# Kernel tuning notes

Measured on AMD Instinct MI355X. Metric: run time of the kernel, lower is better.

The kernel has to match this reference:

```python
import jax, jax.numpy as jnp
import numpy as np

N, D, E, H, K = 16384, 256, 8, 512, 2


def setup_inputs() -> dict:
    key = jax.random.key(0)
    ks = jax.random.split(key, 5)
    inputs = jax.random.normal(ks[0], (N, D), dtype=jnp.float32)
    Wg = jax.random.normal(ks[1], (D, E), dtype=jnp.float32) * 0.05
    w1 = jax.random.normal(ks[2], (E, D, H), dtype=jnp.float32) * 0.05
    b1 = jnp.zeros((E, H), dtype=jnp.float32)
    w2 = jax.random.normal(ks[3], (E, H, D), dtype=jnp.float32) * 0.05
    b2 = jnp.zeros((E, D), dtype=jnp.float32)
    return {"inputs": inputs, "Wg": Wg, "w1": w1, "b1": b1, "w2": w2, "b2": b2}


def reference(inputs, Wg, w1, b1, w2, b2):
    # gate + top-k routing (softmax over the selected logits only, as in the torch code)
    gate_logits = inputs @ Wg                       # [N, E]
    topw, topi = jax.lax.top_k(gate_logits, K)      # [N, K]
    topw = jax.nn.softmax(topw.astype(jnp.float32), axis=1).astype(inputs.dtype)
    # combine weights scattered back into a dense [N, E] matrix (dispatch/combine)
    combine = jnp.zeros((N, E), dtype=inputs.dtype)
    combine = combine.at[jnp.arange(N)[:, None], topi].add(topw)  # [N, E]
    # expert MLP (Linear -> GELU(exact) -> Linear), computed per expert and
    # combined with the sparse routing weights (pool='sum')
    h = jax.nn.gelu(jnp.einsum('nd,edh->neh', inputs, w1) + b1[None], approximate=False)  # [N,E,H]
    y = jnp.einsum('neh,ehd->ned', h, w2) + b2[None]                                      # [N,E,D]
    return jnp.einsum('ne,ned->nd', combine, y)                                           # [N,D]
```

## Files before the change

### kernel.cpp

```cpp
#include <hip/hip_runtime.h>

#define NTOK 16384
#define DIM 256
#define NEXP 8
#define HID 512
#define CAP 5120
#define CSTRIDE 16

typedef unsigned short ushort_t;
typedef short bf16x8 __attribute__((ext_vector_type(8)));
typedef float f32x4 __attribute__((ext_vector_type(4)));

static __device__ __forceinline__ ushort_t f2bf(float f) {
    unsigned int u = __float_as_uint(f);
    unsigned int r = (u + 0x7FFFu + ((u >> 16) & 1u)) >> 16;
    return (ushort_t)r;
}
static __device__ __forceinline__ float bf2f(ushort_t u) {
    unsigned int x = ((unsigned int)u) << 16;
    return __uint_as_float(x);
}
static __device__ __forceinline__ float gelu_fast(float v) {
    float v2 = v * v;
    float u = v * __builtin_fmaf(v2, -0.1029407079f, -2.3022090196f);
    float e = __builtin_amdgcn_exp2f(u);
    return v * __builtin_amdgcn_rcpf(1.0f + e);
}

__global__ void k_transpose(const float* __restrict__ w1, const float* __restrict__ w2,
                            ushort_t* __restrict__ w1t, ushort_t* __restrict__ w2t,
                            int* __restrict__ counts) {
    __shared__ ushort_t tile[64][72];
    if (blockIdx.x == 0 && threadIdx.x < NEXP * CSTRIDE) counts[threadIdx.x] = 0;
    int b = blockIdx.x;
    const float* src; ushort_t* dst; int R, C, e, t;
    if (b < 256) { e = b >> 5; t = b & 31; src = w1; dst = w1t + e * DIM * HID; R = DIM; C = HID; }
    else { b -= 256; e = b >> 5; t = b & 31; src = w2; dst = w2t + e * DIM * HID; R = HID; C = DIM; }
    size_t ebase = (size_t)e * DIM * HID;
    int tilesC = C >> 6;
    int rt = t / tilesC, ct = t % tilesC;
    for (int i = 0; i < 16; i++) {
        int flat = i * 256 + threadIdx.x;
        int lr = flat >> 6, lc = flat & 63;
        tile[lr][lc] = f2bf(src[ebase + (size_t)(rt * 64 + lr) * C + ct * 64 + lc]);
    }
    __syncthreads();
    for (int i = 0; i < 16; i++) {
        int flat = i * 256 + threadIdx.x;
        int lr = flat >> 6, lc = flat & 63;
        dst[(ct * 64 + lr) * R + rt * 64 + lc] = tile[lc][lr];
    }
}

__global__ void k_router(const float* __restrict__ X, const float* __restrict__ Wg,
                         int* counts, int* tok_list, int* inv_idx, float* inv_w,
                         ushort_t* __restrict__ Xb) {
    __shared__ float xs[32][257];
    __shared__ float lg[32][8];
    __shared__ int te0[32], te1[32], lo0[32], lo1[32];
    __shared__ float tw0[32], tw1[32];
    __shared__ int lcnt[NEXP], gbase[NEXP];
    int tid = threadIdx.x;
    int tok0 = blockIdx.x * 32;
    if (tid < NEXP) lcnt[tid] = 0;
    for (int i = 0; i < 4; i++) {
        int flat = i * 256 + tid;
        int r = flat >> 5, c8 = (flat & 31) << 3;
        const float* row = X + (size_t)(tok0 + r) * DIM + c8;
        float4 a = *(const float4*)row;
        float4 b = *(const float4*)(row + 4);
        xs[r][c8 + 0] = a.x; xs[r][c8 + 1] = a.y; xs[r][c8 + 2] = a.z; xs[r][c8 + 3] = a.w;
        xs[r][c8 + 4] = b.x; xs[r][c8 + 5] = b.y; xs[r][c8 + 6] = b.z; xs[r][c8 + 7] = b.w;
    }
    __syncthreads();
    for (int i = 0; i < 4; i++) {
        int flat = i * 256 + tid;
        int r = flat >> 5, c8 = (flat & 31) << 3;
        ushort_t pk[8];
#pragma unroll
        for (int j = 0; j < 8; j++) pk[j] = f2bf(xs[r][c8 + j]);
        *(int4*)(Xb + (size_t)(tok0 + r) * DIM + c8) = *(const int4*)pk;
    }
    int tl = tid & 31, ex = tid >> 5;
    float acc = 0.f;
    for (int d = 0; d < DIM; d++) acc += xs[tl][d] * Wg[d * NEXP + ex];
    lg[tl][ex] = acc;
    __syncthreads();
    if (tid < 32) {
        float best = -1e30f; int bi = 0;
#pragma unroll
        for (int e = 0; e < NEXP; e++) { float v = lg[tid][e]; if (v > best) { best = v; bi = e; } }
        float best2 = -1e30f; int bi2 = 0;
#pragma unroll
        for (int e = 0; e < NEXP; e++) { if (e == bi) continue; float v = lg[tid][e]; if (v > best2) { best2 = v; bi2 = e; } }
        float ed = __expf(best2 - best);
        te0[tid] = bi; te1[tid] = bi2;
        tw0[tid] = 1.0f / (1.0f + ed);
        tw1[tid] = ed / (1.0f + ed);
        lo0[tid] = atomicAdd(&lcnt[bi], 1);
        lo1[tid] = atomicAdd(&lcnt[bi2], 1);
    }
    __syncthreads();
    if (tid < NEXP) gbase[tid] = atomicAdd(&counts[tid * CSTRIDE], lcnt[tid]);
    __syncthreads();
    if (tid < 32) {
        int token = tok0 + tid;
        int e0 = te0[tid], e1 = te1[tid];
        int p0 = gbase[e0] + lo0[tid]; if (p0 >= CAP) p0 = CAP - 1;
        int p1 = gbase[e1] + lo1[tid]; if (p1 >= CAP) p1 = CAP - 1;
        tok_list[e0 * CAP + p0] = token;
        tok_list[e1 * CAP + p1] = token;
        inv_idx[token * 2]     = (e0 << 16) | p0;  inv_w[token * 2]     = tw0[tid];
        inv_idx[token * 2 + 1] = (e1 << 16) | p1;  inv_w[token * 2 + 1] = tw1[tid];
    }
}

__launch_bounds__(512, 4)
__global__ void k_mlp1(const ushort_t* __restrict__ Xb, const ushort_t* __restrict__ w1t,
                       const float* __restrict__ b1,
                       const int* __restrict__ counts, const int* __restrict__ tok_list,
                       ushort_t* __restrict__ hb) {
    __shared__ ushort_t B1[128 * 264];
    int b = blockIdx.x;
    int e = b / 40;
    int tile = b % 40;
    int count = counts[e * CSTRIDE];
    if (count > CAP) count = CAP;
    int t0 = tile * 128;
    if (t0 >= count) return;

    int tid = threadIdx.x;
    int w = tid >> 6, l = tid & 63, ln = l & 15, q = l >> 4;

    int arow = t0 + 16 * w + ln;
    int ci = (arow < count) ? arow : (count - 1);
    int atok = tok_list[e * CAP + ci];
    const ushort_t* xrow = Xb + (size_t)atok * DIM;
    bf16x8 xf[8];
#pragma unroll
    for (int ks = 0; ks < 8; ks++)
        xf[ks] = *(const bf16x8*)(xrow + ks * 32 + q * 8);

    const ushort_t* w1te = w1t + (size_t)e * DIM * HID;
    size_t hrowbase = ((size_t)e * CAP + t0 + 16 * w + ln) * HID;

    for (int hq = 0; hq < 4; hq++) {
        __syncthreads();
#pragma unroll
        for (int i = 0; i < 8; i++) {
            int flat = i * 512 + tid;
            int hr = flat >> 5, c8 = (flat & 31) << 3;
            *(int4*)(B1 + hr * 264 + c8) = *(const int4*)(w1te + (size_t)(hq * 128 + hr) * DIM + c8);
        }
        __syncthreads();

        f32x4 zf = {0.f, 0.f, 0.f, 0.f};
        f32x4 acc[8];
#pragma unroll
        for (int i = 0; i < 8; i++) acc[i] = zf;
#pragma unroll
        for (int ks = 0; ks < 8; ks++) {
            bf16x8 xk = xf[ks];
#pragma unroll
            for (int cf = 0; cf < 8; cf++) {
                bf16x8 wfr = *(const bf16x8*)(B1 + (cf * 16 + ln) * 264 + ks * 32 + q * 8);
                acc[cf] = __builtin_amdgcn_mfma_f32_16x16x32_bf16(wfr, xk, acc[cf], 0, 0, 0);
            }
        }
#pragma unroll
        for (int cf = 0; cf < 8; cf++) {
            float4 bv = *(const float4*)(b1 + e * HID + hq * 128 + cf * 16 + q * 4);
            ushort4 pk;
            pk.x = f2bf(gelu_fast(acc[cf][0] + bv.x));
            pk.y = f2bf(gelu_fast(acc[cf][1] + bv.y));
            pk.z = f2bf(gelu_fast(acc[cf][2] + bv.z));
            pk.w = f2bf(gelu_fast(acc[cf][3] + bv.w));
            *(ushort4*)(hb + hrowbase + hq * 128 + cf * 16 + q * 4) = pk;
        }
    }
}

__launch_bounds__(512, 4)
__global__ void k_mlp2(const ushort_t* __restrict__ hb, const ushort_t* __restrict__ w2t,
                       const float* __restrict__ b2,
                       const int* __restrict__ counts, ushort_t* __restrict__ yb) {
    __shared__ ushort_t B2[64 * 520];
    int b = blockIdx.x;
    int e = b / 40;
    int tile = b % 40;
    int count = counts[e * CSTRIDE];
    if (count > CAP) count = CAP;
    int t0 = tile * 128;
    if (t0 >= count) return;

    int tid = threadIdx.x;
    int w = tid >> 6, l = tid & 63, ln = l & 15, q = l >> 4;

    int arow = t0 + 16 * w + ln;
    int ci = (arow < count) ? arow : (count - 1);
    const ushort_t* hrow = hb + ((size_t)e * CAP + ci) * HID;
    bf16x8 af[16];
#pragma unroll
    for (int ks = 0; ks < 16; ks++)
        af[ks] = *(const bf16x8*)(hrow + ks * 32 + q * 8);

    const ushort_t* w2te = w2t + (size_t)e * DIM * HID;
    size_t yrowbase = ((size_t)e * CAP + t0 + 16 * w + ln) * DIM;

    for (int dq = 0; dq < 4; dq++) {
        __syncthreads();
#pragma unroll
        for (int i = 0; i < 8; i++) {
            int flat = i * 512 + tid;
            int dr = flat >> 6, c8 = (flat & 63) << 3;
            *(int4*)(B2 + dr * 520 + c8) = *(const int4*)(w2te + (size_t)(dq * 64 + dr) * HID + c8);
        }
        __syncthreads();

        f32x4 zf = {0.f, 0.f, 0.f, 0.f};
        f32x4 acc[4];
#pragma unroll
        for (int i = 0; i < 4; i++) acc[i] = zf;
#pragma unroll
        for (int ks = 0; ks < 16; ks++) {
            bf16x8 hk = af[ks];
#pragma unroll
            for (int cf = 0; cf < 4; cf++) {
                bf16x8 wfr = *(const bf16x8*)(B2 + (cf * 16 + ln) * 520 + ks * 32 + q * 8);
                acc[cf] = __builtin_amdgcn_mfma_f32_16x16x32_bf16(wfr, hk, acc[cf], 0, 0, 0);
            }
        }
#pragma unroll
        for (int cf = 0; cf < 4; cf++) {
            float4 bv = *(const float4*)(b2 + e * DIM + dq * 64 + cf * 16 + q * 4);
            ushort4 pk;
            pk.x = f2bf(acc[cf][0] + bv.x);
            pk.y = f2bf(acc[cf][1] + bv.y);
            pk.z = f2bf(acc[cf][2] + bv.z);
            pk.w = f2bf(acc[cf][3] + bv.w);
            *(ushort4*)(yb + yrowbase + dq * 64 + cf * 16 + q * 4) = pk;
        }
    }
}

__global__ void k_combine(const ushort_t* __restrict__ yb, const int* __restrict__ inv_idx,
                          const float* __restrict__ inv_w, float* __restrict__ out) {
    int tid = threadIdx.x;
    int n = blockIdx.x * 8 + (tid >> 5);
    int l32 = tid & 31, c8 = l32 << 3;
    int i0 = inv_idx[2 * n], i1 = inv_idx[2 * n + 1];
    float w0 = inv_w[2 * n], w1 = inv_w[2 * n + 1];
    size_t r0 = (size_t)(i0 >> 16) * CAP + (i0 & 0xFFFF);
    size_t r1 = (size_t)(i1 >> 16) * CAP + (i1 & 0xFFFF);
    int4 v0 = *(const int4*)(yb + r0 * DIM + c8);
    int4 v1 = *(const int4*)(yb + r1 * DIM + c8);
    ushort_t* p0 = (ushort_t*)&v0;
    ushort_t* p1 = (ushort_t*)&v1;
    float4 oa, ob;
    oa.x = w0 * bf2f(p0[0]) + w1 * bf2f(p1[0]);
    oa.y = w0 * bf2f(p0[1]) + w1 * bf2f(p1[1]);
    oa.z = w0 * bf2f(p0[2]) + w1 * bf2f(p1[2]);
    oa.w = w0 * bf2f(p0[3]) + w1 * bf2f(p1[3]);
    ob.x = w0 * bf2f(p0[4]) + w1 * bf2f(p1[4]);
    ob.y = w0 * bf2f(p0[5]) + w1 * bf2f(p1[5]);
    ob.z = w0 * bf2f(p0[6]) + w1 * bf2f(p1[6]);
    ob.w = w0 * bf2f(p0[7]) + w1 * bf2f(p1[7]);
    float4* op = (float4*)(out + (size_t)n * DIM + c8);
    op[0] = oa; op[1] = ob;
}

extern "C" void kernel_launch(void* const* d_in, const int* in_sizes, int n_in,
                              void* d_out, int out_size, void* d_ws, size_t ws_size,
                              hipStream_t stream) {
    const float* X  = (const float*)d_in[0];
    const float* Wg = (const float*)d_in[1];
    const float* w1 = (const float*)d_in[2];
    const float* b1 = (const float*)d_in[3];
    const float* w2 = (const float*)d_in[4];
    const float* b2 = (const float*)d_in[5];

    char* ws = (char*)d_ws;
    size_t off = 0;
    int* counts = (int*)(ws + off);        off = 1024;
    int* tok_list = (int*)(ws + off);      off += (size_t)NEXP * CAP * 4;
    int* inv_idx = (int*)(ws + off);       off += (size_t)NTOK * 2 * 4;
    float* inv_w = (float*)(ws + off);     off += (size_t)NTOK * 2 * 4;
    ushort_t* w1t = (ushort_t*)(ws + off); off += (size_t)NEXP * DIM * HID * 2;
    ushort_t* w2t = (ushort_t*)(ws + off); off += (size_t)NEXP * DIM * HID * 2;
    ushort_t* Xb = (ushort_t*)(ws + off);  off += (size_t)NTOK * DIM * 2;
    ushort_t* hb = (ushort_t*)(ws + off);  off += (size_t)NEXP * CAP * HID * 2;
    ushort_t* yb = (ushort_t*)(ws + off);  off += (size_t)NEXP * CAP * DIM * 2;

    k_transpose<<<512, 256, 0, stream>>>(w1, w2, w1t, w2t, counts);
    k_router<<<512, 256, 0, stream>>>(X, Wg, counts, tok_list, inv_idx, inv_w, Xb);
    k_mlp1<<<NEXP * 40, 512, 0, stream>>>(Xb, w1t, b1, counts, tok_list, hb);
    k_mlp2<<<NEXP * 40, 512, 0, stream>>>(hb, w2t, b2, counts, yb);
    k_combine<<<2048, 256, 0, stream>>>(yb, inv_idx, inv_w, (float*)d_out);
}
```

Measured before the change: 183.8 us.

## Split MLP kernels across output-column chunks for more, smaller blocks

Each MLP block now handles 64 token rows and a single 64-wide (mlp1) or 32-wide (mlp2) output column chunk, with the chunk index taken from the grid. This replaces the in-block loop over four column chunks. Grid size grows from 320 to 5120 blocks of 256 threads, with smaller shared tiles, to raise occupancy and spread load across CUs. The cost is that each block reloads its activation rows, so gathered X and h reads are repeated 8 times, and more blocks exit early.

```diff
diff --git a/kernel.cpp b/kernel.cpp
--- a/kernel.cpp
+++ b/kernel.cpp
@@ -115,18 +115,19 @@
     }
 }
 
-__launch_bounds__(512, 4)
+__launch_bounds__(256, 4)
 __global__ void k_mlp1(const ushort_t* __restrict__ Xb, const ushort_t* __restrict__ w1t,
                        const float* __restrict__ b1,
                        const int* __restrict__ counts, const int* __restrict__ tok_list,
                        ushort_t* __restrict__ hb) {
-    __shared__ ushort_t B1[128 * 264];
+    __shared__ ushort_t B1[64 * 264];
     int b = blockIdx.x;
-    int e = b / 40;
-    int tile = b % 40;
+    int e = b / 640;
+    int rem = b % 640;
+    int hq = rem / 80, tile = rem % 80;
     int count = counts[e * CSTRIDE];
     if (count > CAP) count = CAP;
-    int t0 = tile * 128;
+    int t0 = tile * 64;
     if (t0 >= count) return;
 
     int tid = threadIdx.x;
@@ -141,56 +142,53 @@
     for (int ks = 0; ks < 8; ks++)
         xf[ks] = *(const bf16x8*)(xrow + ks * 32 + q * 8);
 
-    const ushort_t* w1te = w1t + (size_t)e * DIM * HID;
-    size_t hrowbase = ((size_t)e * CAP + t0 + 16 * w + ln) * HID;
-
-    for (int hq = 0; hq < 4; hq++) {
-        __syncthreads();
-#pragma unroll
-        for (int i = 0; i < 8; i++) {
-            int flat = i * 512 + tid;
-            int hr = flat >> 5, c8 = (flat & 31) << 3;
-            *(int4*)(B1 + hr * 264 + c8) = *(const int4*)(w1te + (size_t)(hq * 128 + hr) * DIM + c8);
+    const ushort_t* w1te = w1t + (size_t)e * DIM * HID + (size_t)hq * 64 * DIM;
+#pragma unroll
+    for (int i = 0; i < 8; i++) {
+        int flat = i * 256 + tid;
+        int hr = flat >> 5, c8 = (flat & 31) << 3;
+        *(int4*)(B1 + hr * 264 + c8) = *(const int4*)(w1te + hr * DIM + c8);
+    }
+    __syncthreads();
+
+    f32x4 zf = {0.f, 0.f, 0.f, 0.f};
+    f32x4 acc[4];
+#pragma unroll
+    for (int i = 0; i < 4; i++) acc[i] = zf;
+#pragma unroll
+    for (int ks = 0; ks < 8; ks++) {
+        bf16x8 xk = xf[ks];
+#pragma unroll
+        for (int cf = 0; cf < 4; cf++) {
+            bf16x8 wfr = *(const bf16x8*)(B1 + (cf * 16 + ln) * 264 + ks * 32 + q * 8);
+            acc[cf] = __builtin_amdgcn_mfma_f32_16x16x32_bf16(wfr, xk, acc[cf], 0, 0, 0);
         }
-        __syncthreads();
-
-        f32x4 zf = {0.f, 0.f, 0.f, 0.f};
-        f32x4 acc[8];
-#pragma unroll
-        for (int i = 0; i < 8; i++) acc[i] = zf;
-#pragma unroll
-        for (int ks = 0; ks < 8; ks++) {
-            bf16x8 xk = xf[ks];
-#pragma unroll
-            for (int cf = 0; cf < 8; cf++) {
-                bf16x8 wfr = *(const bf16x8*)(B1 + (cf * 16 + ln) * 264 + ks * 32 + q * 8);
-                acc[cf] = __builtin_amdgcn_mfma_f32_16x16x32_bf16(wfr, xk, acc[cf], 0, 0, 0);
-            }
-        }
-#pragma unroll
-        for (int cf = 0; cf < 8; cf++) {
-            float4 bv = *(const float4*)(b1 + e * HID + hq * 128 + cf * 16 + q * 4);
-            ushort4 pk;
-            pk.x = f2bf(gelu_fast(acc[cf][0] + bv.x));
-            pk.y = f2bf(gelu_fast(acc[cf][1] + bv.y));
-            pk.z = f2bf(gelu_fast(acc[cf][2] + bv.z));
-            pk.w = f2bf(gelu_fast(acc[cf][3] + bv.w));
-            *(ushort4*)(hb + hrowbase + hq * 128 + cf * 16 + q * 4) = pk;
-        }
-    }
-}
-
-__launch_bounds__(512, 4)
+    }
+    size_t hrowbase = ((size_t)e * CAP + arow) * HID + hq * 64;
+#pragma unroll
+    for (int cf = 0; cf < 4; cf++) {
+        float4 bv = *(const float4*)(b1 + e * HID + hq * 64 + cf * 16 + q * 4);
+        ushort4 pk;
+        pk.x = f2bf(gelu_fast(acc[cf][0] + bv.x));
+        pk.y = f2bf(gelu_fast(acc[cf][1] + bv.y));
+        pk.z = f2bf(gelu_fast(acc[cf][2] + bv.z));
+        pk.w = f2bf(gelu_fast(acc[cf][3] + bv.w));
+        *(ushort4*)(hb + hrowbase + cf * 16 + q * 4) = pk;
+    }
+}
+
+__launch_bounds__(256, 4)
 __global__ void k_mlp2(const ushort_t* __restrict__ hb, const ushort_t* __restrict__ w2t,
                        const float* __restrict__ b2,
                        const int* __restrict__ counts, ushort_t* __restrict__ yb) {
-    __shared__ ushort_t B2[64 * 520];
+    __shared__ ushort_t B2[32 * 520];
     int b = blockIdx.x;
-    int e = b / 40;
-    int tile = b % 40;
+    int e = b / 640;
+    int rem = b % 640;
+    int dq = rem / 80, tile = rem % 80;
     int count = counts[e * CSTRIDE];
     if (count > CAP) count = CAP;
-    int t0 = tile * 128;
+    int t0 = tile * 64;
     if (t0 >= count) return;
 
     int tid = threadIdx.x;
@@ -204,42 +202,37 @@
     for (int ks = 0; ks < 16; ks++)
         af[ks] = *(const bf16x8*)(hrow + ks * 32 + q * 8);
 
-    const ushort_t* w2te = w2t + (size_t)e * DIM * HID;
-    size_t yrowbase = ((size_t)e * CAP + t0 + 16 * w + ln) * DIM;
-
-    for (int dq = 0; dq < 4; dq++) {
-        __syncthreads();
-#pragma unroll
-        for (int i = 0; i < 8; i++) {
-            int flat = i * 512 + tid;
-            int dr = flat >> 6, c8 = (flat & 63) << 3;
-            *(int4*)(B2 + dr * 520 + c8) = *(const int4*)(w2te + (size_t)(dq * 64 + dr) * HID + c8);
+    const ushort_t* w2te = w2t + (size_t)e * DIM * HID + (size_t)dq * 32 * HID;
+#pragma unroll
+    for (int i = 0; i < 8; i++) {
+        int flat = i * 256 + tid;
+        int dr = flat >> 6, c8 = (flat & 63) << 3;
+        *(int4*)(B2 + dr * 520 + c8) = *(const int4*)(w2te + dr * HID + c8);
+    }
+    __syncthreads();
+
+    f32x4 zf = {0.f, 0.f, 0.f, 0.f};
+    f32x4 acc[2];
+    acc[0] = zf; acc[1] = zf;
+#pragma unroll
+    for (int ks = 0; ks < 16; ks++) {
+        bf16x8 hk = af[ks];
+#pragma unroll
+        for (int cf = 0; cf < 2; cf++) {
+            bf16x8 wfr = *(const bf16x8*)(B2 + (cf * 16 + ln) * 520 + ks * 32 + q * 8);
+            acc[cf] = __builtin_amdgcn_mfma_f32_16x16x32_bf16(wfr, hk, acc[cf], 0, 0, 0);
         }
-        __syncthreads();
-
-        f32x4 zf = {0.f, 0.f, 0.f, 0.f};
-        f32x4 acc[4];
-#pragma unroll
-        for (int i = 0; i < 4; i++) acc[i] = zf;
-#pragma unroll
-        for (int ks = 0; ks < 16; ks++) {
-            bf16x8 hk = af[ks];
-#pragma unroll
-            for (int cf = 0; cf < 4; cf++) {
-                bf16x8 wfr = *(const bf16x8*)(B2 + (cf * 16 + ln) * 520 + ks * 32 + q * 8);
-                acc[cf] = __builtin_amdgcn_mfma_f32_16x16x32_bf16(wfr, hk, acc[cf], 0, 0, 0);
-            }
-        }
-#pragma unroll
-        for (int cf = 0; cf < 4; cf++) {
-            float4 bv = *(const float4*)(b2 + e * DIM + dq * 64 + cf * 16 + q * 4);
-            ushort4 pk;
-            pk.x = f2bf(acc[cf][0] + bv.x);
-            pk.y = f2bf(acc[cf][1] + bv.y);
-            pk.z = f2bf(acc[cf][2] + bv.z);
-            pk.w = f2bf(acc[cf][3] + bv.w);
-            *(ushort4*)(yb + yrowbase + dq * 64 + cf * 16 + q * 4) = pk;
-        }
+    }
+    size_t yrowbase = ((size_t)e * CAP + arow) * DIM + dq * 32;
+#pragma unroll
+    for (int cf = 0; cf < 2; cf++) {
+        float4 bv = *(const float4*)(b2 + e * DIM + dq * 32 + cf * 16 + q * 4);
+        ushort4 pk;
+        pk.x = f2bf(acc[cf][0] + bv.x);
+        pk.y = f2bf(acc[cf][1] + bv.y);
+        pk.z = f2bf(acc[cf][2] + bv.z);
+        pk.w = f2bf(acc[cf][3] + bv.w);
+        *(ushort4*)(yb + yrowbase + cf * 16 + q * 4) = pk;
     }
 }
 
@@ -293,7 +286,7 @@
 
     k_transpose<<<512, 256, 0, stream>>>(w1, w2, w1t, w2t, counts);
     k_router<<<512, 256, 0, stream>>>(X, Wg, counts, tok_list, inv_idx, inv_w, Xb);
-    k_mlp1<<<NEXP * 40, 512, 0, stream>>>(Xb, w1t, b1, counts, tok_list, hb);
-    k_mlp2<<<NEXP * 40, 512, 0, stream>>>(hb, w2t, b2, counts, yb);
+    k_mlp1<<<NEXP * 8 * 80, 256, 0, stream>>>(Xb, w1t, b1, counts, tok_list, hb);
+    k_mlp2<<<NEXP * 8 * 80, 256, 0, stream>>>(hb, w2t, b2, counts, yb);
     k_combine<<<2048, 256, 0, stream>>>(yb, inv_idx, inv_w, (float*)d_out);
 }
```

Result: faster. 178.0 us (-3.2%).
